# Optimization experiments

Measured on AMD Instinct MI355X. Metric: run time of the kernel, lower is better.

## Reference

```python
import jax, jax.numpy as jnp
import numpy as np
import math

B, T, C = 4, 2048, 1024
NH, D = 16, 64


def setup_inputs() -> dict:
    key = jax.random.key(0)
    ks = jax.random.split(key, 7)
    s = 0.02
    return {
        "x": jax.random.normal(ks[0], (B, T, C), dtype=jnp.float32),
        "W_attn": jax.random.normal(ks[1], (C, 3 * C), dtype=jnp.float32) * s,
        "b_attn": jax.random.normal(ks[2], (3 * C,), dtype=jnp.float32) * s,
        "W_proj": jax.random.normal(ks[3], (C, C), dtype=jnp.float32) * s,
        "b_proj": jax.random.normal(ks[4], (C,), dtype=jnp.float32) * s,
        # bQ/bK emulate mean_Q + std_Q*randn (resampled biases), broadcast over heads
        "bQ": 0.5 + 0.1 * jax.random.normal(ks[5], (NH, D), dtype=jnp.float32),
        "bK": 0.3 + 0.1 * jax.random.normal(ks[6], (NH, D), dtype=jnp.float32),
    }


def reference(x, W_attn, b_attn, W_proj, b_proj, bQ, bK):
    b, t, c = x.shape
    nh, d = bQ.shape
    qkv = x @ W_attn + b_attn                       # [B,T,3C]
    q, k, v = jnp.split(qkv, 3, axis=2)
    # [B,T,C] -> [B,nh,T,d]
    q = q.reshape(b, t, nh, d).transpose(0, 2, 1, 3)
    k = k.reshape(b, t, nh, d).transpose(0, 2, 1, 3)
    v = v.reshape(b, t, nh, d).transpose(0, 2, 1, 3)
    q = q + bQ[None, :, None, :]
    k = k + bK[None, :, None, :]
    scores = jnp.einsum('bhqd,bhkd->bhqk', q, k) / math.sqrt(d)
    causal = jnp.tril(jnp.ones((t, t), dtype=bool))
    scores = jnp.where(causal[None, None], scores, jnp.finfo(scores.dtype).min)
    att = jax.nn.softmax(scores, axis=-1)
    y = jnp.einsum('bhqk,bhkd->bhqd', att, v)       # [B,nh,T,d]
    y = y.transpose(0, 2, 1, 3).reshape(b, t, c)
    out = y @ W_proj + b_proj
    return (out, bQ)
```

## Files before the change

### kernel.cpp

```cpp
#include <hip/hip_runtime.h>
#include <hip/hip_bf16.h>

#define B_  4
#define T_  2048
#define C_  1024
#define NH_ 16
#define D_  64
#define BH_ (B_*NH_)
#define M_  (B_*T_)

typedef __attribute__((ext_vector_type(8))) short short8;
typedef __attribute__((ext_vector_type(4))) short short4v;
typedef __attribute__((ext_vector_type(4))) float f32x4;

#define SC2 0.18033688011112043f

__device__ __forceinline__ ushort f2bf(float f) {
    unsigned u = __float_as_uint(f);
    u += 0x7FFF + ((u >> 16) & 1);
    return (ushort)(u >> 16);
}

__device__ __forceinline__ unsigned cvtpk(float lo, float hi) {
    unsigned r;
    asm("v_cvt_pk_bf16_f32 %0, %1, %2" : "=v"(r) : "v"(lo), "v"(hi));
    return r;
}

__device__ __forceinline__ void gload16(const void* g, void* lds) {
    __builtin_amdgcn_global_load_lds(
        (const __attribute__((address_space(1))) void*)g,
        (__attribute__((address_space(3))) void*)lds, 16, 0, 0);
}

__global__ __launch_bounds__(256) void prepass_kernel(
    const float* __restrict__ x, ushort* __restrict__ Xb,
    const float* __restrict__ Wa, ushort* __restrict__ Wat,
    const float* __restrict__ bQ, float* __restrict__ bqDst)
{
    __shared__ float t[64][65];
    const int bid = blockIdx.x;
    const int tid = threadIdx.x;

    if (bid < 2048) {
        const int n8 = M_*C_/8;
        const int stride = 2048 * 256;
        for (int idx = bid*256 + tid; idx < n8; idx += stride) {
            const float* p = x + (size_t)idx * 8;
            f32x4 a = *(const f32x4*)p;
            f32x4 b = *(const f32x4*)(p + 4);
            union { short8 v; ushort u[8]; } pk;
            #pragma unroll
            for (int j = 0; j < 4; ++j) { pk.u[j] = f2bf(a[j]); pk.u[4+j] = f2bf(b[j]); }
            *(short8*)&Xb[(size_t)idx * 8] = pk.v;
        }
    } else if (bid < 2816) {
        const int tb = bid - 2048;
        const int n0 = (tb % 48) * 64;
        const int k0 = (tb / 48) * 64;
        const int K = C_, N = 3*C_;
        #pragma unroll
        for (int it = 0; it < 16; ++it) {
            const int kr = it*4 + (tid >> 6);
            t[kr][tid & 63] = Wa[(size_t)(k0 + kr) * N + n0 + (tid & 63)];
        }
        __syncthreads();
        const int nr8 = tid >> 3;
        const int kc0 = (tid & 7) * 8;
        #pragma unroll
        for (int j = 0; j < 2; ++j) {
            const int nr = j*32 + nr8;
            union { short8 v; ushort u[8]; } pk;
            #pragma unroll
            for (int e = 0; e < 8; ++e) pk.u[e] = f2bf(t[kc0 + e][nr]);
            *(short8*)&Wat[(size_t)(n0 + nr) * K + k0 + kc0] = pk.v;
        }
    } else {
        for (int i = tid; i < NH_*D_; i += 256) bqDst[i] = bQ[i];
    }
}

__global__ __launch_bounds__(256) void transpose_w_kernel(
    const float* __restrict__ in, ushort* __restrict__ out, int K, int N)
{
    __shared__ float t[64][65];
    const int tid = threadIdx.x;
    const int n0 = blockIdx.x * 64;
    const int k0 = blockIdx.y * 64;
    #pragma unroll
    for (int it = 0; it < 16; ++it) {
        const int kr = it*4 + (tid >> 6);
        t[kr][tid & 63] = in[(size_t)(k0 + kr) * N + n0 + (tid & 63)];
    }
    __syncthreads();
    const int nr8 = tid >> 3;
    const int kc0 = (tid & 7) * 8;
    #pragma unroll
    for (int j = 0; j < 2; ++j) {
        const int nr = j*32 + nr8;
        union { short8 v; ushort u[8]; } pk;
        #pragma unroll
        for (int e = 0; e < 8; ++e) pk.u[e] = f2bf(t[kc0 + e][nr]);
        *(short8*)&out[(size_t)(n0 + nr) * K + k0 + kc0] = pk.v;
    }
}

template<int MODE>
__global__ __launch_bounds__(256) void gemm128_kernel(
    const ushort* __restrict__ A, const ushort* __restrict__ Bt,
    const float* __restrict__ b_attn, const float* __restrict__ bQv,
    const float* __restrict__ bKv,
    ushort* __restrict__ Qb, ushort* __restrict__ Kb, ushort* __restrict__ Vt,
    float* __restrict__ outp, const float* __restrict__ b_proj,
    int K, int N)
{
    __shared__ ushort SH[24576];

    const int tid  = threadIdx.x;
    const int lane = tid & 63;
    const int w    = tid >> 6;
    const int wr   = w >> 1, wc = w & 1;
    const int l16  = lane & 15, lg = lane >> 4;

    const int bid = blockIdx.x;
    const int xcd = bid & 7;
    const int idx = bid >> 3;
    const int m0  = (xcd*8 + (idx & 7)) * 128;
    const int n0  = (idx >> 3) * 128;

    const int srow = lane >> 2;
    const int scol = (lane & 3) * 8;
    const ushort* aS = A  + (size_t)(m0 + w*32 + srow) * K + scol;
    const ushort* bS = Bt + (size_t)(n0 + w*32 + srow) * K + scol;

    f32x4 acc[4][4] = {};

    const int NT = K >> 5;

    #define STAGE(tk, bi)                                                     \
        do {                                                                  \
            const int kn_ = (tk) * 32;                                        \
            gload16(aS + kn_,                SH + (bi)*4096 + w*1024);        \
            gload16(aS + (size_t)16*K + kn_, SH + (bi)*4096 + w*1024 + 512);  \
            gload16(bS + kn_,                SH + 12288 + (bi)*4096 + w*1024);\
            gload16(bS + (size_t)16*K + kn_, SH + 12288 + (bi)*4096 + w*1024 + 512);\
        } while (0)

    STAGE(0, 0);
    STAGE(1, 1);
    asm volatile("s_waitcnt vmcnt(4)" ::: "memory");
    __builtin_amdgcn_s_barrier();

    for (int t = 0; t < NT; ++t) {
        const int cur = t % 3;
        if (t + 2 < NT)
            STAGE(t + 2, (t + 2) % 3);

        short8 af[4], bf[4];
        #pragma unroll
        for (int i = 0; i < 4; ++i) {
            af[i] = *(const short8*)&SH[cur*4096 + (wr*64 + i*16 + l16)*32 + lg*8];
            bf[i] = *(const short8*)&SH[12288 + cur*4096 + (wc*64 + i*16 + l16)*32 + lg*8];
        }
        #pragma unroll
        for (int mi = 0; mi < 4; ++mi)
            #pragma unroll
            for (int ni = 0; ni < 4; ++ni)
                acc[mi][ni] = __builtin_amdgcn_mfma_f32_16x16x32_bf16(
                    af[mi], bf[ni], acc[mi][ni], 0, 0, 0);

        if (t + 1 < NT) {
            if (t + 2 < NT)
                asm volatile("s_waitcnt vmcnt(4)" ::: "memory");
            else
                asm volatile("s_waitcnt vmcnt(0)" ::: "memory");
            __builtin_amdgcn_s_barrier();
        }
    }
    #undef STAGE

    if constexpr (MODE == 0) {
        if (n0 >= 2048) {
            __syncthreads();
            ushort* TL = SH;
            #pragma unroll
            for (int ni = 0; ni < 4; ++ni) {
                const int nl = wc*64 + ni*16 + l16;
                const float ba = b_attn[n0 + nl];
                #pragma unroll
                for (int mi = 0; mi < 4; ++mi)
                    #pragma unroll
                    for (int r = 0; r < 4; ++r) {
                        const int ml = wr*64 + mi*16 + lg*4 + r;
                        TL[nl*136 + ml] = f2bf(acc[mi][ni][r] + ba);
                    }
            }
            __syncthreads();
            const int bblk = m0 >> 11;
            const int tblk = m0 & 2047;
            const int h0   = (n0 & 1023) >> 6;
            #pragma unroll
            for (int it = 0; it < 8; ++it) {
                const int row = w*32 + it*4 + (lane >> 4);
                const int d   = row & 63;
                const int h   = h0 + (row >> 6);
                const short8 v = *(const short8*)&TL[row*136 + (lane & 15)*8];
                *(short8*)(Vt + ((size_t)(bblk*NH_ + h)*D_ + d)*T_ + tblk + (lane & 15)*8) = v;
            }
        } else {
            #pragma unroll
            for (int ni = 0; ni < 4; ++ni) {
                const int n = n0 + wc*64 + ni*16 + l16;
                const int sec = n >> 10;
                const int nn  = n & 1023;
                const int h = nn >> 6, d = nn & 63;
                const float ba = b_attn[n];
                #pragma unroll
                for (int mi = 0; mi < 4; ++mi) {
                    #pragma unroll
                    for (int r = 0; r < 4; ++r) {
                        const int m = m0 + wr*64 + mi*16 + lg*4 + r;
                        const int b = m >> 11, t = m & 2047;
                        float v = acc[mi][ni][r] + ba;
                        if (sec == 0) {
                            v = (v + bQv[nn]) * SC2;
                            Qb[((size_t)(b*NH_ + h)*T_ + t)*D_ + d] = f2bf(v);
                        } else {
                            v += bKv[nn];
                            Kb[((size_t)(b*NH_ + h)*T_ + t)*D_ + d] = f2bf(v);
                        }
                    }
                }
            }
        }
    } else {
        #pragma unroll
        for (int ni = 0; ni < 4; ++ni) {
            const int n = n0 + wc*64 + ni*16 + l16;
            const float bp = b_proj[n];
            #pragma unroll
            for (int mi = 0; mi < 4; ++mi)
                #pragma unroll
                for (int r = 0; r < 4; ++r) {
                    const int m = m0 + wr*64 + mi*16 + lg*4 + r;
                    outp[(size_t)m * N + n] = acc[mi][ni][r] + bp;
                }
        }
    }
}

__global__ __launch_bounds__(256, 5) void attn_kernel(
    const ushort* __restrict__ Qb, const ushort* __restrict__ Kb,
    const ushort* __restrict__ Vt, ushort* __restrict__ y)
{
    __shared__ char lds[2][16384];

    const int tid  = threadIdx.x;
    const int lane = tid & 63;
    const int w    = tid >> 6;
    const int l16  = lane & 15, lg = lane >> 4;
    const int bid  = blockIdx.x;
    const int xcd  = bid & 7;
    const int idx  = bid >> 3;
    const int bh   = (xcd << 3) | (idx & 7);
    const int p    = 31 - (idx >> 3);
    const int b    = bh >> 4, h = bh & 15;
    const size_t kvb = (size_t)bh * T_ * D_;
    const size_t vtb = (size_t)bh * D_ * T_;

    int srow[2], scol[2];
    #pragma unroll
    for (int i = 0; i < 2; ++i) {
        const int l = w*2048 + i*1024 + lane*16;
        const int r = l >> 7;
        const int c = (l & 127) ^ ((r & 7) << 4);
        srow[i] = r; scol[i] = c >> 1;
    }

    const f32x4 z4 = {0.f, 0.f, 0.f, 0.f};

    const int qw = p * 64 + w * 16;

    short8 qf[2];
    #pragma unroll
    for (int c = 0; c < 2; ++c)
        qf[c] = *(const short8*)(Qb + kvb +
                    (size_t)(qw + l16)*D_ + c*32 + lg*8);

    f32x4 o[4] = {};
    float mrow = -1e30f;
    float lrow = 0.f;
    const int nt = p + 1;

    #pragma unroll
    for (int i = 0; i < 2; ++i) {
        gload16(Kb + kvb + (size_t)srow[i]*D_ + scol[i],
                &lds[0][w*2048 + i*1024]);
        gload16(Vt + vtb + (size_t)srow[i]*T_ + scol[i],
                &lds[0][8192 + w*2048 + i*1024]);
    }

    #pragma unroll 1
    for (int t = 0; t < nt; ++t) {
        const int kb = t * 64;
        if (t + 1 < nt) {
            char* Lb = lds[(t + 1) & 1];
            const int kb1 = kb + 64;
            #pragma unroll
            for (int i = 0; i < 2; ++i) {
                gload16(Kb + kvb + (size_t)(kb1 + srow[i])*D_ + scol[i],
                        Lb + w*2048 + i*1024);
                gload16(Vt + vtb + (size_t)srow[i]*T_ + kb1 + scol[i],
                        Lb + 8192 + w*2048 + i*1024);
            }
            asm volatile("s_waitcnt vmcnt(4)" ::: "memory");
        } else {
            asm volatile("s_waitcnt vmcnt(0)" ::: "memory");
        }
        __builtin_amdgcn_s_barrier();

        {
            const char* Lk = lds[t & 1];
            const char* Lv = lds[t & 1] + 8192;

            f32x4 s[4];
            #pragma unroll
            for (int t4 = 0; t4 < 4; ++t4) {
                const int r = t4*16 + l16;
                const int m = (r & 7) << 4;
                const short8 kc0 = *(const short8*)(Lk + r*128 + (( lg*16     ) ^ m));
                const short8 kc1 = *(const short8*)(Lk + r*128 + ((64 + lg*16 ) ^ m));
                s[t4] = __builtin_amdgcn_mfma_f32_16x16x32_bf16(kc0, qf[0], z4,    0, 0, 0);
                s[t4] = __builtin_amdgcn_mfma_f32_16x16x32_bf16(kc1, qf[1], s[t4], 0, 0, 0);
            }

            const bool full = (kb + 63 <= qw);
            float x[4][4];
            #pragma unroll
            for (int t4 = 0; t4 < 4; ++t4)
                #pragma unroll
                for (int r = 0; r < 4; ++r) {
                    float v = s[t4][r];
                    if (!full)
                        v = (kb + t4*16 + lg*4 + r <= qw + l16) ? v : -1e30f;
                    x[t4][r] = v;
                }
            float vm0 = fmaxf(fmaxf(x[0][0], x[0][1]), fmaxf(x[0][2], x[0][3]));
            float vm1 = fmaxf(fmaxf(x[1][0], x[1][1]), fmaxf(x[1][2], x[1][3]));
            float vm2 = fmaxf(fmaxf(x[2][0], x[2][1]), fmaxf(x[2][2], x[2][3]));
            float vm3 = fmaxf(fmaxf(x[3][0], x[3][1]), fmaxf(x[3][2], x[3][3]));
            float vm  = fmaxf(fmaxf(vm0, vm1), fmaxf(vm2, vm3));
            vm = fmaxf(vm, __shfl_xor(vm, 16, 64));
            vm = fmaxf(vm, __shfl_xor(vm, 32, 64));
            const float mn = fmaxf(mrow, vm);
            float rs = 0.f;
            #pragma unroll
            for (int t4 = 0; t4 < 4; ++t4)
                #pragma unroll
                for (int r = 0; r < 4; ++r) {
                    const float pe = __builtin_amdgcn_exp2f(x[t4][r] - mn);
                    x[t4][r] = pe;
                    rs += pe;
                }
            rs += __shfl_xor(rs, 16, 64);
            rs += __shfl_xor(rs, 32, 64);
            if (__all(vm <= mrow)) {
                lrow += rs;
            } else {
                const float al = __builtin_amdgcn_exp2f(mrow - mn);
                lrow = lrow*al + rs;
                #pragma unroll
                for (int cb = 0; cb < 4; ++cb)
                    #pragma unroll
                    for (int r = 0; r < 4; ++r)
                        o[cb][r] *= al;
            }
            mrow = mn;

            union { unsigned u[4]; short8 v; } p0, p1;
            p0.u[0] = cvtpk(x[0][0], x[0][1]);
            p0.u[1] = cvtpk(x[0][2], x[0][3]);
            p0.u[2] = cvtpk(x[1][0], x[1][1]);
            p0.u[3] = cvtpk(x[1][2], x[1][3]);
            p1.u[0] = cvtpk(x[2][0], x[2][1]);
            p1.u[1] = cvtpk(x[2][2], x[2][3]);
            p1.u[2] = cvtpk(x[3][0], x[3][1]);
            p1.u[3] = cvtpk(x[3][2], x[3][3]);

            #pragma unroll
            for (int cb = 0; cb < 4; ++cb) {
                const int d = cb*16 + l16;
                const int mv = (d & 7) << 4;
                const char* vb = Lv + d*128;
                union { short8 v; short4v hh[2]; } v0, v1;
                v0.hh[0] = *(const short4v*)(vb + ((lg*8     ) ^ mv));
                v0.hh[1] = *(const short4v*)(vb + ((lg*8 + 32) ^ mv));
                v1.hh[0] = *(const short4v*)(vb + ((lg*8 + 64) ^ mv));
                v1.hh[1] = *(const short4v*)(vb + ((lg*8 + 96) ^ mv));
                o[cb] = __builtin_amdgcn_mfma_f32_16x16x32_bf16(v0.v, p0.v, o[cb], 0, 0, 0);
                o[cb] = __builtin_amdgcn_mfma_f32_16x16x32_bf16(v1.v, p1.v, o[cb], 0, 0, 0);
            }
        }
        __builtin_amdgcn_s_barrier();
    }

    {
        const float inv = 1.0f / lrow;
        const int q = qw + l16;
        ushort* yr = y + ((size_t)b*T_ + q)*C_ + h*D_ + lg*4;
        #pragma unroll
        for (int cb = 0; cb < 4; ++cb) {
            union { unsigned u[2]; short4v v; } st;
            st.u[0] = cvtpk(o[cb][0]*inv, o[cb][1]*inv);
            st.u[1] = cvtpk(o[cb][2]*inv, o[cb][3]*inv);
            *(short4v*)(yr + cb*16) = st.v;
        }
    }
}

extern "C" void kernel_launch(void* const* d_in, const int* in_sizes, int n_in,
                              void* d_out, int out_size, void* d_ws, size_t ws_size,
                              hipStream_t stream)
{
    const float* x      = (const float*)d_in[0];
    const float* W_attn = (const float*)d_in[1];
    const float* b_attn = (const float*)d_in[2];
    const float* W_proj = (const float*)d_in[3];
    const float* b_proj = (const float*)d_in[4];
    const float* bQ     = (const float*)d_in[5];
    const float* bK     = (const float*)d_in[6];
    float* out = (float*)d_out;

    const size_t HE = (size_t)BH_ * T_ * D_;
    ushort* Qb = (ushort*)d_ws;
    ushort* Kb = Qb + HE;
    ushort* Vt = Kb + HE;
    ushort* y  = Vt + HE;
    ushort* Wpt = (ushort*)d_ws;

    ushort* Xb  = (ushort*)d_out;
    ushort* Wat = (ushort*)d_out + (size_t)M_ * C_;

    prepass_kernel<<<2817, 256, 0, stream>>>(x, Xb, W_attn, Wat,
                                             bQ, out + (size_t)M_ * C_);

    gemm128_kernel<0><<<1536, 256, 0, stream>>>(
        Xb, Wat, b_attn, bQ, bK, Qb, Kb, Vt, nullptr, nullptr, C_, 3*C_);

    attn_kernel<<<2048, 256, 0, stream>>>(Qb, Kb, Vt, y);

    transpose_w_kernel<<<dim3(C_/64, C_/64), 256, 0, stream>>>(W_proj, Wpt, C_, C_);

    gemm128_kernel<1><<<512, 256, 0, stream>>>(
        y, Wpt, nullptr, nullptr, nullptr, nullptr, nullptr, nullptr,
        out, b_proj, C_, C_);
}
```

Before: 200.0 us.

## Use 256x256 tiles with 8 waves and swizzled LDS for the QKV GEMM

Replaces the 128x128, 256-thread QKV projection GEMM with a dedicated 256x256-tile kernel of 512 threads. It uses a 64-wide K step split into two halves, double buffering, XOR-swizzled LDS addressing, and s_setprio around the MFMA bursts. The larger tile raises arithmetic intensity and cuts global and LDS traffic per FLOP, and the swizzle is meant to avoid bank conflicts. In exchange it needs 128KB of LDS and many more accumulator registers, and the grid shrinks to 384 blocks, so occupancy is low and tail imbalance across CUs is possible. The output projection GEMM becomes a separate non-templated kernel with unchanged logic.

```diff
diff --git a/kernel.cpp b/kernel.cpp
--- a/kernel.cpp
+++ b/kernel.cpp
@@ -105,12 +105,204 @@
     }
 }
 
-template<int MODE>
-__global__ __launch_bounds__(256) void gemm128_kernel(
+__global__ __launch_bounds__(512, 2) void gemmqkv_kernel(
     const ushort* __restrict__ A, const ushort* __restrict__ Bt,
     const float* __restrict__ b_attn, const float* __restrict__ bQv,
     const float* __restrict__ bKv,
-    ushort* __restrict__ Qb, ushort* __restrict__ Kb, ushort* __restrict__ Vt,
+    ushort* __restrict__ Qb, ushort* __restrict__ Kb, ushort* __restrict__ Vt)
+{
+    __shared__ ushort SH[65536];
+
+    const int K = C_;
+    const int NT = 16;
+    const int tid  = threadIdx.x;
+    const int lane = tid & 63;
+    const int w    = tid >> 6;
+    const int wr   = w >> 2;
+    const int wc   = w & 3;
+    const int l16  = lane & 15, lg = lane >> 4;
+
+    const int bid = blockIdx.x;
+    const int xcd = bid & 7;
+    const int idx = bid >> 3;
+    const int m0  = (xcd*4 + (idx & 3)) * 256;
+    const int n0  = (idx >> 2) * 256;
+
+    const int gsw = 8 * ((lane & 3) ^ ((lane >> 3) & 3));
+    const ushort* aBase = A  + (size_t)(m0 + w*32 + (lane >> 2)) * K + gsw;
+    const ushort* bBase = Bt + (size_t)(n0 + w*32 + (lane >> 2)) * K + gsw;
+    const int fsw = ((lg ^ ((l16 >> 1) & 3)) << 3);
+
+    f32x4 acc[8][4] = {};
+
+    #define STG_A(tk, kh)                                                     \
+        do { ushort* d_ = SH + ((tk)&1)*16384 + (kh)*8192 + w*1024;           \
+             const ushort* s_ = aBase + (tk)*64 + (kh)*32;                    \
+             gload16(s_, d_); gload16(s_ + 16*K, d_ + 512); } while (0)
+    #define STG_B(tk, kh)                                                     \
+        do { ushort* d_ = SH + 32768 + ((tk)&1)*16384 + (kh)*8192 + w*1024;   \
+             const ushort* s_ = bBase + (tk)*64 + (kh)*32;                    \
+             gload16(s_, d_); gload16(s_ + 16*K, d_ + 512); } while (0)
+    #define BAR()   __builtin_amdgcn_s_barrier()
+    #define LGKM()  do { asm volatile("s_waitcnt lgkmcnt(0)" ::: "memory");   \
+                         __builtin_amdgcn_sched_barrier(0); } while (0)
+    #define VMC4()  asm volatile("s_waitcnt vmcnt(4)" ::: "memory")
+    #define VMC0()  asm volatile("s_waitcnt vmcnt(0)" ::: "memory")
+
+    STG_A(0, 0); STG_B(0, 0); STG_A(0, 1); STG_B(0, 1);
+    VMC4();
+    BAR();
+
+    #pragma unroll 1
+    for (int t = 0; t < NT; ++t) {
+        const int cb = (t & 1) * 16384;
+        const bool st = (t + 1 < NT);
+        short8 bf[4], af[4];
+
+        {
+            const ushort* Ah = SH + cb;
+            const ushort* Bh = SH + 32768 + cb;
+            #pragma unroll
+            for (int ni = 0; ni < 4; ++ni)
+                bf[ni] = *(const short8*)&Bh[(wc*64 + ni*16 + l16)*32 + fsw];
+            #pragma unroll
+            for (int q = 0; q < 4; ++q)
+                af[q] = *(const short8*)&Ah[(wr*128 + q*16 + l16)*32 + fsw];
+            if (st) STG_A(t + 1, 0);
+            BAR(); LGKM();
+            __builtin_amdgcn_s_setprio(1);
+            #pragma unroll
+            for (int q = 0; q < 4; ++q)
+                #pragma unroll
+                for (int ni = 0; ni < 4; ++ni)
+                    acc[q][ni] = __builtin_amdgcn_mfma_f32_16x16x32_bf16(
+                        af[q], bf[ni], acc[q][ni], 0, 0, 0);
+            __builtin_amdgcn_s_setprio(0);
+            BAR();
+        }
+        {
+            const ushort* Ah = SH + cb;
+            #pragma unroll
+            for (int q = 0; q < 4; ++q)
+                af[q] = *(const short8*)&Ah[(wr*128 + (4+q)*16 + l16)*32 + fsw];
+            if (st) STG_B(t + 1, 0);
+            BAR(); LGKM();
+            __builtin_amdgcn_s_setprio(1);
+            #pragma unroll
+            for (int q = 0; q < 4; ++q)
+                #pragma unroll
+                for (int ni = 0; ni < 4; ++ni)
+                    acc[4+q][ni] = __builtin_amdgcn_mfma_f32_16x16x32_bf16(
+                        af[q], bf[ni], acc[4+q][ni], 0, 0, 0);
+            __builtin_amdgcn_s_setprio(0);
+            if (st) VMC4(); else VMC0();
+            BAR();
+        }
+        {
+            const ushort* Ah = SH + cb + 8192;
+            const ushort* Bh = SH + 32768 + cb + 8192;
+            #pragma unroll
+            for (int ni = 0; ni < 4; ++ni)
+                bf[ni] = *(const short8*)&Bh[(wc*64 + ni*16 + l16)*32 + fsw];
+            #pragma unroll
+            for (int q = 0; q < 4; ++q)
+                af[q] = *(const short8*)&Ah[(wr*128 + q*16 + l16)*32 + fsw];
+            if (st) STG_A(t + 1, 1);
+            BAR(); LGKM();
+            __builtin_amdgcn_s_setprio(1);
+            #pragma unroll
+            for (int q = 0; q < 4; ++q)
+                #pragma unroll
+                for (int ni = 0; ni < 4; ++ni)
+                    acc[q][ni] = __builtin_amdgcn_mfma_f32_16x16x32_bf16(
+                        af[q], bf[ni], acc[q][ni], 0, 0, 0);
+            __builtin_amdgcn_s_setprio(0);
+            BAR();
+        }
+        {
+            const ushort* Ah = SH + cb + 8192;
+            #pragma unroll
+            for (int q = 0; q < 4; ++q)
+                af[q] = *(const short8*)&Ah[(wr*128 + (4+q)*16 + l16)*32 + fsw];
+            if (st) STG_B(t + 1, 1);
+            BAR(); LGKM();
+            __builtin_amdgcn_s_setprio(1);
+            #pragma unroll
+            for (int q = 0; q < 4; ++q)
+                #pragma unroll
+                for (int ni = 0; ni < 4; ++ni)
+                    acc[4+q][ni] = __builtin_amdgcn_mfma_f32_16x16x32_bf16(
+                        af[q], bf[ni], acc[4+q][ni], 0, 0, 0);
+            __builtin_amdgcn_s_setprio(0);
+            if (st) VMC4();
+            BAR();
+        }
+    }
+    #undef STG_A
+    #undef STG_B
+
+    if (n0 < 2048) {
+        #pragma unroll
+        for (int ni = 0; ni < 4; ++ni) {
+            const int n = n0 + wc*64 + ni*16 + l16;
+            const int sec = n >> 10;
+            const int nn  = n & 1023;
+            const int h = nn >> 6, d = nn & 63;
+            const float ba = b_attn[n];
+            #pragma unroll
+            for (int mi = 0; mi < 8; ++mi) {
+                #pragma unroll
+                for (int r = 0; r < 4; ++r) {
+                    const int m = m0 + wr*128 + mi*16 + lg*4 + r;
+                    const int b = m >> 11, tt = m & 2047;
+                    float v = acc[mi][ni][r] + ba;
+                    if (sec == 0) {
+                        v = (v + bQv[nn]) * SC2;
+                        Qb[((size_t)(b*NH_ + h)*T_ + tt)*D_ + d] = f2bf(v);
+                    } else {
+                        v += bKv[nn];
+                        Kb[((size_t)(b*NH_ + h)*T_ + tt)*D_ + d] = f2bf(v);
+                    }
+                }
+            }
+        }
+    } else {
+        ushort* TL = SH;
+        const int bblk = m0 >> 11;
+        const int tcol0 = m0 & 2047;
+        const int h0 = (n0 & 1023) >> 6;
+        #pragma unroll 1
+        for (int mh = 0; mh < 2; ++mh) {
+            __syncthreads();
+            if (wr == mh) {
+                #pragma unroll
+                for (int ni = 0; ni < 4; ++ni) {
+                    const int nl = wc*64 + ni*16 + l16;
+                    const float ba = b_attn[n0 + nl];
+                    #pragma unroll
+                    for (int mi = 0; mi < 8; ++mi)
+                        #pragma unroll
+                        for (int r = 0; r < 4; ++r)
+                            TL[nl*132 + mi*16 + lg*4 + r] =
+                                f2bf(acc[mi][ni][r] + ba);
+                }
+            }
+            __syncthreads();
+            #pragma unroll
+            for (int it = 0; it < 8; ++it) {
+                const int row = w*32 + it*4 + lg;
+                const int d = row & 63;
+                const int h = h0 + (row >> 6);
+                const short8 v = *(const short8*)&TL[row*132 + l16*8];
+                *(short8*)(Vt + ((size_t)(bblk*NH_ + h)*D_ + d)*T_
+                           + tcol0 + mh*128 + l16*8) = v;
+            }
+        }
+    }
+}
+
+__global__ __launch_bounds__(256) void gemm2_kernel(
+    const ushort* __restrict__ A, const ushort* __restrict__ Bt,
     float* __restrict__ outp, const float* __restrict__ b_proj,
     int K, int N)
 {
@@ -134,7 +326,6 @@
     const ushort* bS = Bt + (size_t)(n0 + w*32 + srow) * K + scol;
 
     f32x4 acc[4][4] = {};
-
     const int NT = K >> 5;
 
     #define STAGE(tk, bi)                                                     \
@@ -179,73 +370,17 @@
     }
     #undef STAGE
 
-    if constexpr (MODE == 0) {
-        if (n0 >= 2048) {
-            __syncthreads();
-            ushort* TL = SH;
-            #pragma unroll
-            for (int ni = 0; ni < 4; ++ni) {
-                const int nl = wc*64 + ni*16 + l16;
-                const float ba = b_attn[n0 + nl];
-                #pragma unroll
-                for (int mi = 0; mi < 4; ++mi)
-                    #pragma unroll
-                    for (int r = 0; r < 4; ++r) {
-                        const int ml = wr*64 + mi*16 + lg*4 + r;
-                        TL[nl*136 + ml] = f2bf(acc[mi][ni][r] + ba);
-                    }
-            }
-            __syncthreads();
-            const int bblk = m0 >> 11;
-            const int tblk = m0 & 2047;
-            const int h0   = (n0 & 1023) >> 6;
-            #pragma unroll
-            for (int it = 0; it < 8; ++it) {
-                const int row = w*32 + it*4 + (lane >> 4);
-                const int d   = row & 63;
-                const int h   = h0 + (row >> 6);
-                const short8 v = *(const short8*)&TL[row*136 + (lane & 15)*8];
-                *(short8*)(Vt + ((size_t)(bblk*NH_ + h)*D_ + d)*T_ + tblk + (lane & 15)*8) = v;
-            }
-        } else {
-            #pragma unroll
-            for (int ni = 0; ni < 4; ++ni) {
-                const int n = n0 + wc*64 + ni*16 + l16;
-                const int sec = n >> 10;
-                const int nn  = n & 1023;
-                const int h = nn >> 6, d = nn & 63;
-                const float ba = b_attn[n];
-                #pragma unroll
-                for (int mi = 0; mi < 4; ++mi) {
-                    #pragma unroll
-                    for (int r = 0; r < 4; ++r) {
-                        const int m = m0 + wr*64 + mi*16 + lg*4 + r;
-                        const int b = m >> 11, t = m & 2047;
-                        float v = acc[mi][ni][r] + ba;
-                        if (sec == 0) {
-                            v = (v + bQv[nn]) * SC2;
-                            Qb[((size_t)(b*NH_ + h)*T_ + t)*D_ + d] = f2bf(v);
-                        } else {
-                            v += bKv[nn];
-                            Kb[((size_t)(b*NH_ + h)*T_ + t)*D_ + d] = f2bf(v);
-                        }
-                    }
-                }
-            }
-        }
-    } else {
-        #pragma unroll
-        for (int ni = 0; ni < 4; ++ni) {
-            const int n = n0 + wc*64 + ni*16 + l16;
-            const float bp = b_proj[n];
-            #pragma unroll
-            for (int mi = 0; mi < 4; ++mi)
-                #pragma unroll
-                for (int r = 0; r < 4; ++r) {
-                    const int m = m0 + wr*64 + mi*16 + lg*4 + r;
-                    outp[(size_t)m * N + n] = acc[mi][ni][r] + bp;
-                }
-        }
+    #pragma unroll
+    for (int ni = 0; ni < 4; ++ni) {
+        const int n = n0 + wc*64 + ni*16 + l16;
+        const float bp = b_proj[n];
+        #pragma unroll
+        for (int mi = 0; mi < 4; ++mi)
+            #pragma unroll
+            for (int r = 0; r < 4; ++r) {
+                const int m = m0 + wr*64 + mi*16 + lg*4 + r;
+                outp[(size_t)m * N + n] = acc[mi][ni][r] + bp;
+            }
     }
 }
 
@@ -444,14 +579,13 @@
     prepass_kernel<<<2817, 256, 0, stream>>>(x, Xb, W_attn, Wat,
                                              bQ, out + (size_t)M_ * C_);
 
-    gemm128_kernel<0><<<1536, 256, 0, stream>>>(
-        Xb, Wat, b_attn, bQ, bK, Qb, Kb, Vt, nullptr, nullptr, C_, 3*C_);
+    gemmqkv_kernel<<<384, 512, 0, stream>>>(
+        Xb, Wat, b_attn, bQ, bK, Qb, Kb, Vt);
 
     attn_kernel<<<2048, 256, 0, stream>>>(Qb, Kb, Vt, y);
 
     transpose_w_kernel<<<dim3(C_/64, C_/64), 256, 0, stream>>>(W_proj, Wpt, C_, C_);
 
-    gemm128_kernel<1><<<512, 256, 0, stream>>>(
-        y, Wpt, nullptr, nullptr, nullptr, nullptr, nullptr, nullptr,
-        out, b_proj, C_, C_);
-}
+    gemm2_kernel<<<512, 256, 0, stream>>>(
+        y, Wpt, out, b_proj, C_, C_);
+}
```

Result: no change. 197.1 us (-1.4%).
